# Kernel optimization log

Measured on AMD Instinct MI355X. Metric: run time of the kernel, lower is better.

The kernel has to match this reference:

```python
import jax, jax.numpy as jnp
import numpy as np

PATCH_LEN = 16
D_MODEL = 512


def setup_inputs() -> dict:
    key = jax.random.key(0)
    k_x, k_w1, k_b1, k_w2, k_b2 = jax.random.split(key, 5)
    x = jax.random.normal(k_x, (8, 32, 512), dtype=jnp.float32)
    # Filter_Generators: Linear(patch_len -> d_model), ReLU, Linear(d_model -> patch_len*d_model), ReLU
    s1 = 1.0 / np.sqrt(PATCH_LEN)
    s2 = 1.0 / np.sqrt(D_MODEL)
    W1 = jax.random.uniform(k_w1, (PATCH_LEN, D_MODEL), jnp.float32, -s1, s1)
    b1 = jax.random.uniform(k_b1, (D_MODEL,), jnp.float32, -s1, s1)
    W2 = jax.random.uniform(k_w2, (D_MODEL, PATCH_LEN * D_MODEL), jnp.float32, -s2, s2)
    b2 = jax.random.uniform(k_b2, (PATCH_LEN * D_MODEL,), jnp.float32, -s2, s2)
    return {"x": x, "W1": W1, "b1": b1, "W2": W2, "b2": b2}


def reference(x, W1, b1, W2, b2):
    B = x.shape[0]
    # reshape to patches: (B, N, patch_len)
    xp = x.reshape(B, -1, PATCH_LEN)
    N = xp.shape[1]
    # dynamic filter generation MLP
    h = jax.nn.relu(jnp.einsum('bnp,pd->bnd', xp, W1) + b1)          # (B,N,D)
    filt = jax.nn.relu(jnp.einsum('bnd,de->bne', h, W2) + b2)        # (B,N,P*D)
    # softmax over the sequence (N) axis, per channel (dim=-2 in torch)
    filt = jax.nn.softmax(filt, axis=1)
    filt = filt.reshape(B, N, D_MODEL, PATCH_LEN)                    # (B,N,D,P)
    # broadcast multiply with input patches
    out = filt * xp[:, :, None, :]                                   # (B,N,D,P)
    out = out.transpose(0, 1, 3, 2).reshape(B, N * PATCH_LEN, D_MODEL)
    # AvgPool1d(kernel=3, stride=1, padding=1, count_include_pad=True) over last dim
    p = jnp.pad(out, ((0, 0), (0, 0), (1, 1)))
    out = (p[..., :-2] + p[..., 1:-1] + p[..., 2:]) * (1.0 / 3.0)
    return out
```

## Files before the change

### kernel.cpp

```cpp
#include <hip/hip_runtime.h>
#include <stdint.h>

typedef __attribute__((ext_vector_type(8))) short short8;
typedef __attribute__((ext_vector_type(4))) float floatx4;
typedef unsigned short ushort_t;

__device__ __forceinline__ ushort_t f2bf(float f) {
    union { float f; unsigned int i; } v; v.f = f;
    unsigned int r = v.i + 0x7fffu + ((v.i >> 16) & 1u);
    return (ushort_t)(r >> 16);
}


__global__ __launch_bounds__(256) void k_prep(
    const float* __restrict__ W2, ushort_t* __restrict__ W2T)
{
    __shared__ float t[32][33];
    const int tid = threadIdx.x;
    const int tx = tid & 31, ty = tid >> 5;
    const int e0 = blockIdx.x * 32, k0 = blockIdx.y * 32;
#pragma unroll
    for (int i = 0; i < 4; ++i)
        t[ty + i * 8][tx] = W2[(size_t)(k0 + ty + i * 8) * 8192 + e0 + tx];
    __syncthreads();
#pragma unroll
    for (int i = 0; i < 4; ++i)
        W2T[(size_t)(e0 + ty + i * 8) * 512 + k0 + tx] = f2bf(t[tx][ty + i * 8]);
}

__global__ __launch_bounds__(256) void k1_hidden(
    const float* __restrict__ x, const float* __restrict__ W1,
    const float* __restrict__ b1, ushort_t* __restrict__ h)
{
    __shared__ float xs[16];
    const int r = blockIdx.x;
    const int tid = threadIdx.x;
    if (tid < 16) xs[tid] = x[r * 16 + tid];
    __syncthreads();
#pragma unroll
    for (int dd = 0; dd < 2; ++dd) {
        int d = tid + dd * 256;
        float s = b1[d];
#pragma unroll
        for (int p = 0; p < 16; ++p)
            s += xs[p] * W1[p * 512 + d];
        s = s > 0.f ? s : 0.f;
        h[(size_t)r * 512 + d] = f2bf(s);
    }
}

__global__ __launch_bounds__(256) void k2_sums(
    const ushort_t* __restrict__ h,
    const ushort_t* __restrict__ W2T,
    const float* __restrict__ b2,
    float* __restrict__ P)
{
    __shared__ __align__(16) ushort_t As[128 * 32];
    __shared__ __align__(16) ushort_t Bs[128 * 32];
    __shared__ float csum[128];
    const int tid = threadIdx.x;
    const int lane = tid & 63;
    const int wave = tid >> 6;
    const int quad = lane >> 4;
    const int l16 = lane & 15;
    const int i0 = blockIdx.x * 128;
    const int e0 = blockIdx.y * 128;
    const int wr = (wave >> 1) * 64;
    const int wc = (wave & 1) * 64;

    if (tid < 128) csum[tid] = 0.f;

    floatx4 acc[4][4];
#pragma unroll
    for (int i = 0; i < 4; ++i)
#pragma unroll
        for (int j = 0; j < 4; ++j)
            acc[i][j] = (floatx4){0.f, 0.f, 0.f, 0.f};

    for (int k0 = 0; k0 < 512; k0 += 32) {
#pragma unroll
        for (int s = 0; s < 2; ++s) {
            int q = tid + s * 256;
            int row = q >> 2;
            int c = q & 3;
            uint4 va = *reinterpret_cast<const uint4*>(&h[(size_t)(i0 + row) * 512 + k0 + c * 8]);
            uint4 vb = *reinterpret_cast<const uint4*>(&W2T[(size_t)(e0 + row) * 512 + k0 + c * 8]);
            *reinterpret_cast<uint4*>(&As[row * 32 + ((c ^ (row & 3)) << 3)]) = va;
            *reinterpret_cast<uint4*>(&Bs[row * 32 + ((c ^ (row & 3)) << 3)]) = vb;
        }
        __syncthreads();
        short8 af[4], bf[4];
#pragma unroll
        for (int i = 0; i < 4; ++i) {
            int m = wr + i * 16 + l16;
            af[i] = *reinterpret_cast<const short8*>(&As[m * 32 + ((quad ^ (m & 3)) << 3)]);
            int n = wc + i * 16 + l16;
            bf[i] = *reinterpret_cast<const short8*>(&Bs[n * 32 + ((quad ^ (n & 3)) << 3)]);
        }
#pragma unroll
        for (int i = 0; i < 4; ++i)
#pragma unroll
            for (int j = 0; j < 4; ++j)
                acc[i][j] = __builtin_amdgcn_mfma_f32_16x16x32_bf16(af[i], bf[j], acc[i][j], 0, 0, 0);
        __syncthreads();
    }

#pragma unroll
    for (int j = 0; j < 4; ++j) {
        int eg = e0 + wc + j * 16 + l16;
        float b2v = b2[eg];
        float csj = 0.f;
#pragma unroll
        for (int i = 0; i < 4; ++i)
#pragma unroll
            for (int r = 0; r < 4; ++r) {
                float v = acc[i][j][r] + b2v;
                v = v > 0.f ? v : 0.f;
                csj += __expf(v);
            }
        csj += __shfl_xor(csj, 16, 64);
        csj += __shfl_xor(csj, 32, 64);
        if (lane < 16) atomicAdd(&csum[wc + j * 16 + l16], csj);
    }
    __syncthreads();
    if (tid < 128) P[(size_t)blockIdx.x * 8192 + e0 + tid] = csum[tid];
}

__global__ __launch_bounds__(256) void k_rdenom(const float* __restrict__ P,
                                                float* __restrict__ rden)
{
    int idx = blockIdx.x * 256 + threadIdx.x;
    int b = idx >> 13;
    int e = idx & 8191;
    float s = 0.f;
#pragma unroll
    for (int j = 0; j < 8; ++j) s += P[(size_t)(b * 8 + j) * 8192 + e];
    rden[idx] = 1.0f / s;
}

__global__ __launch_bounds__(256) void k2_final(
    const ushort_t* __restrict__ h,
    const ushort_t* __restrict__ W2T,
    const float* __restrict__ b2,
    const float* __restrict__ x,
    const float* __restrict__ rden,
    float* __restrict__ out)
{
    __shared__ __align__(16) ushort_t As[128 * 32];
    __shared__ __align__(16) ushort_t Bs[160 * 32];
    __shared__ float xs[128 * 17];
    const int tid = threadIdx.x;
    const int lane = tid & 63;
    const int wave = tid >> 6;
    const int quad = lane >> 4;
    const int l16 = lane & 15;
    const int i0 = blockIdx.x * 128;
    const int d0 = blockIdx.y * 8;
    const int ebase = blockIdx.y * 128 - 16;
    const int wrow = wave * 32;
    const int b = i0 >> 10;

#pragma unroll
    for (int s = 0; s < 8; ++s) {
        int q = tid + s * 256;
        xs[(q >> 4) * 17 + (q & 15)] = x[(size_t)(i0 + (q >> 4)) * 16 + (q & 15)];
    }

    floatx4 acc[2][10];
#pragma unroll
    for (int i = 0; i < 2; ++i)
#pragma unroll
        for (int t = 0; t < 10; ++t)
            acc[i][t] = (floatx4){0.f, 0.f, 0.f, 0.f};

    for (int k0 = 0; k0 < 512; k0 += 32) {
#pragma unroll
        for (int s = 0; s < 2; ++s) {
            int q = tid + s * 256;
            int row = q >> 2, c = q & 3;
            uint4 va = *reinterpret_cast<const uint4*>(&h[(size_t)(i0 + row) * 512 + k0 + c * 8]);
            *reinterpret_cast<uint4*>(&As[row * 32 + ((c ^ (row & 3)) << 3)]) = va;
        }
#pragma unroll
        for (int s = 0; s < 3; ++s) {
            int q = tid + s * 256;
            if (q < 640) {
                int row = q >> 2, c = q & 3;
                int eg = ebase + row;
                eg = eg < 0 ? 0 : (eg > 8191 ? 8191 : eg);
                uint4 vb = *reinterpret_cast<const uint4*>(&W2T[(size_t)eg * 512 + k0 + c * 8]);
                *reinterpret_cast<uint4*>(&Bs[row * 32 + ((c ^ (row & 3)) << 3)]) = vb;
            }
        }
        __syncthreads();
        short8 af[2], bf[10];
#pragma unroll
        for (int i = 0; i < 2; ++i) {
            int m = wrow + i * 16 + l16;
            af[i] = *reinterpret_cast<const short8*>(&As[m * 32 + ((quad ^ (m & 3)) << 3)]);
        }
#pragma unroll
        for (int t = 0; t < 10; ++t) {
            int n = t * 16 + l16;
            bf[t] = *reinterpret_cast<const short8*>(&Bs[n * 32 + ((quad ^ (n & 3)) << 3)]);
        }
#pragma unroll
        for (int i = 0; i < 2; ++i)
#pragma unroll
            for (int t = 0; t < 10; ++t)
                acc[i][t] = __builtin_amdgcn_mfma_f32_16x16x32_bf16(af[i], bf[t], acc[i][t], 0, 0, 0);
        __syncthreads();
    }

#pragma unroll
    for (int t = 0; t < 10; ++t) {
        int el = t * 16 + l16;
        int eg = ebase + el;
        int valid = (eg >= 0) & (eg < 8192);
        int egc = valid ? eg : 0;
        float b2v = b2[egc];
        float scale = valid ? rden[b * 8192 + egc] : 0.f;
#pragma unroll
        for (int i = 0; i < 2; ++i) {
            int rbase = wrow + i * 16 + quad * 4;
#pragma unroll
            for (int r = 0; r < 4; ++r) {
                float v = acc[i][t][r] + b2v;
                v = v > 0.f ? v : 0.f;
                acc[i][t][r] = __expf(v) * scale * xs[(rbase + r) * 17 + l16];
            }
        }
    }

    const float inv3 = 1.f / 3.f;
#pragma unroll
    for (int i = 0; i < 2; ++i) {
        int rbase = wrow + i * 16 + quad * 4;
#pragma unroll
        for (int r = 0; r < 4; ++r) {
            int row = rbase + r;
            float g0 = acc[i][0][r], g1 = acc[i][1][r], g2 = acc[i][2][r];
            float g3 = acc[i][3][r], g4 = acc[i][4][r], g5 = acc[i][5][r];
            float g6 = acc[i][6][r], g7 = acc[i][7][r], g8 = acc[i][8][r];
            float g9 = acc[i][9][r];
            float4 o1, o2;
            o1.x = (g0 + g1 + g2) * inv3;
            o1.y = (g1 + g2 + g3) * inv3;
            o1.z = (g2 + g3 + g4) * inv3;
            o1.w = (g3 + g4 + g5) * inv3;
            o2.x = (g4 + g5 + g6) * inv3;
            o2.y = (g5 + g6 + g7) * inv3;
            o2.z = (g6 + g7 + g8) * inv3;
            o2.w = (g7 + g8 + g9) * inv3;
            size_t orow = (size_t)((i0 + row) * 16 + l16);
            *reinterpret_cast<float4*>(&out[orow * 512 + d0]) = o1;
            *reinterpret_cast<float4*>(&out[orow * 512 + d0 + 4]) = o2;
        }
    }
}

extern "C" void kernel_launch(void* const* d_in, const int* in_sizes, int n_in,
                              void* d_out, int out_size, void* d_ws, size_t ws_size,
                              hipStream_t stream)
{
    const float* x  = (const float*)d_in[0];
    const float* W1 = (const float*)d_in[1];
    const float* b1 = (const float*)d_in[2];
    const float* W2 = (const float*)d_in[3];
    const float* b2 = (const float*)d_in[4];
    float* out = (float*)d_out;

    char* ws = (char*)d_ws;
    ushort_t* h    = (ushort_t*)(ws);
    ushort_t* W2T  = (ushort_t*)(ws + (size_t)(8u << 20));
    float*    rden = (float*)(ws + (size_t)(16u << 20));
    float*    P    = (float*)d_out;

    k_prep<<<dim3(256, 16), 256, 0, stream>>>(W2, W2T);
    k1_hidden<<<8192, 256, 0, stream>>>(x, W1, b1, h);
    k2_sums<<<dim3(64, 64), 256, 0, stream>>>(h, W2T, b2, P);
    k_rdenom<<<256, 256, 0, stream>>>(P, rden);
    k2_final<<<dim3(64, 64), 256, 0, stream>>>(h, W2T, b2, x, rden, out);
}
```

Baseline: 597.5 us.

## Double-buffer LDS tiles in both GEMM kernels and load x into registers

Both MFMA GEMM kernels (k2_sums and k2_final) now use two LDS buffers. The next K-tile's global loads are issued into registers before the current tile's MFMAs and written to the other buffer afterwards, which leaves one barrier per iteration. The goal is to hide global load latency behind compute. k2_final also drops its xs shared array and reads x values straight into registers after the main loop. The cost is twice the LDS footprint, which may reduce occupancy, plus more register pressure from the staged loads.

After: 584.9 us. -2.1%, faster.

```diff
diff --git a/kernel.cpp b/kernel.cpp
--- a/kernel.cpp
+++ b/kernel.cpp
@@ -55,8 +55,8 @@
     const float* __restrict__ b2,
     float* __restrict__ P)
 {
-    __shared__ __align__(16) ushort_t As[128 * 32];
-    __shared__ __align__(16) ushort_t Bs[128 * 32];
+    __shared__ __align__(16) ushort_t As[2][128 * 32];
+    __shared__ __align__(16) ushort_t Bs[2][128 * 32];
     __shared__ float csum[128];
     const int tid = threadIdx.x;
     const int lane = tid & 63;
@@ -70,6 +70,16 @@
 
     if (tid < 128) csum[tid] = 0.f;
 
+    const int q0 = tid, q1 = tid + 256;
+    const int row0 = q0 >> 2, c0 = q0 & 3;
+    const int row1 = q1 >> 2, c1 = q1 & 3;
+    const int w0 = row0 * 32 + ((c0 ^ (row0 & 3)) << 3);
+    const int w1 = row1 * 32 + ((c1 ^ (row1 & 3)) << 3);
+    const ushort_t* gA0 = &h[(size_t)(i0 + row0) * 512 + c0 * 8];
+    const ushort_t* gA1 = &h[(size_t)(i0 + row1) * 512 + c1 * 8];
+    const ushort_t* gB0 = &W2T[(size_t)(e0 + row0) * 512 + c0 * 8];
+    const ushort_t* gB1 = &W2T[(size_t)(e0 + row1) * 512 + c1 * 8];
+
     floatx4 acc[4][4];
 #pragma unroll
     for (int i = 0; i < 4; ++i)
@@ -77,32 +87,47 @@
         for (int j = 0; j < 4; ++j)
             acc[i][j] = (floatx4){0.f, 0.f, 0.f, 0.f};
 
-    for (int k0 = 0; k0 < 512; k0 += 32) {
-#pragma unroll
-        for (int s = 0; s < 2; ++s) {
-            int q = tid + s * 256;
-            int row = q >> 2;
-            int c = q & 3;
-            uint4 va = *reinterpret_cast<const uint4*>(&h[(size_t)(i0 + row) * 512 + k0 + c * 8]);
-            uint4 vb = *reinterpret_cast<const uint4*>(&W2T[(size_t)(e0 + row) * 512 + k0 + c * 8]);
-            *reinterpret_cast<uint4*>(&As[row * 32 + ((c ^ (row & 3)) << 3)]) = va;
-            *reinterpret_cast<uint4*>(&Bs[row * 32 + ((c ^ (row & 3)) << 3)]) = vb;
-        }
-        __syncthreads();
-        short8 af[4], bf[4];
+    uint4 a0 = *reinterpret_cast<const uint4*>(gA0);
+    uint4 a1 = *reinterpret_cast<const uint4*>(gA1);
+    uint4 b0 = *reinterpret_cast<const uint4*>(gB0);
+    uint4 b1 = *reinterpret_cast<const uint4*>(gB1);
+    *reinterpret_cast<uint4*>(&As[0][w0]) = a0;
+    *reinterpret_cast<uint4*>(&As[0][w1]) = a1;
+    *reinterpret_cast<uint4*>(&Bs[0][w0]) = b0;
+    *reinterpret_cast<uint4*>(&Bs[0][w1]) = b1;
+    __syncthreads();
+
+    int cur = 0;
+    for (int kt = 0; kt < 16; ++kt) {
+        uint4 na0, na1, nb0, nb1;
+        if (kt < 15) {
+            int k0 = (kt + 1) * 32;
+            na0 = *reinterpret_cast<const uint4*>(gA0 + k0);
+            na1 = *reinterpret_cast<const uint4*>(gA1 + k0);
+            nb0 = *reinterpret_cast<const uint4*>(gB0 + k0);
+            nb1 = *reinterpret_cast<const uint4*>(gB1 + k0);
+        }
+        short8 af[4], bfr[4];
 #pragma unroll
         for (int i = 0; i < 4; ++i) {
             int m = wr + i * 16 + l16;
-            af[i] = *reinterpret_cast<const short8*>(&As[m * 32 + ((quad ^ (m & 3)) << 3)]);
+            af[i] = *reinterpret_cast<const short8*>(&As[cur][m * 32 + ((quad ^ (m & 3)) << 3)]);
             int n = wc + i * 16 + l16;
-            bf[i] = *reinterpret_cast<const short8*>(&Bs[n * 32 + ((quad ^ (n & 3)) << 3)]);
+            bfr[i] = *reinterpret_cast<const short8*>(&Bs[cur][n * 32 + ((quad ^ (n & 3)) << 3)]);
         }
 #pragma unroll
         for (int i = 0; i < 4; ++i)
 #pragma unroll
             for (int j = 0; j < 4; ++j)
-                acc[i][j] = __builtin_amdgcn_mfma_f32_16x16x32_bf16(af[i], bf[j], acc[i][j], 0, 0, 0);
+                acc[i][j] = __builtin_amdgcn_mfma_f32_16x16x32_bf16(af[i], bfr[j], acc[i][j], 0, 0, 0);
+        if (kt < 15) {
+            *reinterpret_cast<uint4*>(&As[cur ^ 1][w0]) = na0;
+            *reinterpret_cast<uint4*>(&As[cur ^ 1][w1]) = na1;
+            *reinterpret_cast<uint4*>(&Bs[cur ^ 1][w0]) = nb0;
+            *reinterpret_cast<uint4*>(&Bs[cur ^ 1][w1]) = nb1;
+        }
         __syncthreads();
+        cur ^= 1;
     }
 
 #pragma unroll
@@ -146,9 +171,8 @@
     const float* __restrict__ rden,
     float* __restrict__ out)
 {
-    __shared__ __align__(16) ushort_t As[128 * 32];
-    __shared__ __align__(16) ushort_t Bs[160 * 32];
-    __shared__ float xs[128 * 17];
+    __shared__ __align__(16) ushort_t As[2][128 * 32];
+    __shared__ __align__(16) ushort_t Bs[2][160 * 32];
     const int tid = threadIdx.x;
     const int lane = tid & 63;
     const int wave = tid >> 6;
@@ -160,11 +184,22 @@
     const int wrow = wave * 32;
     const int b = i0 >> 10;
 
-#pragma unroll
-    for (int s = 0; s < 8; ++s) {
-        int q = tid + s * 256;
-        xs[(q >> 4) * 17 + (q & 15)] = x[(size_t)(i0 + (q >> 4)) * 16 + (q & 15)];
-    }
+    const int q0 = tid, q1 = tid + 256, q2 = tid + 512;
+    const int row0 = q0 >> 2, c0 = q0 & 3;
+    const int row1 = q1 >> 2, c1 = q1 & 3;
+    const int row2 = q2 >> 2, c2 = q2 & 3;
+    const bool act2 = q2 < 640;
+    const int w0 = row0 * 32 + ((c0 ^ (row0 & 3)) << 3);
+    const int w1 = row1 * 32 + ((c1 ^ (row1 & 3)) << 3);
+    const int w2 = row2 * 32 + ((c2 ^ (row2 & 3)) << 3);
+    int ebr0 = ebase + row0; ebr0 = ebr0 < 0 ? 0 : (ebr0 > 8191 ? 8191 : ebr0);
+    int ebr1 = ebase + row1; ebr1 = ebr1 < 0 ? 0 : (ebr1 > 8191 ? 8191 : ebr1);
+    int ebr2 = ebase + row2; ebr2 = ebr2 < 0 ? 0 : (ebr2 > 8191 ? 8191 : ebr2);
+    const ushort_t* gA0 = &h[(size_t)(i0 + row0) * 512 + c0 * 8];
+    const ushort_t* gA1 = &h[(size_t)(i0 + row1) * 512 + c1 * 8];
+    const ushort_t* gB0 = &W2T[(size_t)ebr0 * 512 + c0 * 8];
+    const ushort_t* gB1 = &W2T[(size_t)ebr1 * 512 + c1 * 8];
+    const ushort_t* gB2 = &W2T[(size_t)ebr2 * 512 + c2 * 8];
 
     floatx4 acc[2][10];
 #pragma unroll
@@ -173,44 +208,66 @@
         for (int t = 0; t < 10; ++t)
             acc[i][t] = (floatx4){0.f, 0.f, 0.f, 0.f};
 
-    for (int k0 = 0; k0 < 512; k0 += 32) {
-#pragma unroll
-        for (int s = 0; s < 2; ++s) {
-            int q = tid + s * 256;
-            int row = q >> 2, c = q & 3;
-            uint4 va = *reinterpret_cast<const uint4*>(&h[(size_t)(i0 + row) * 512 + k0 + c * 8]);
-            *reinterpret_cast<uint4*>(&As[row * 32 + ((c ^ (row & 3)) << 3)]) = va;
-        }
-#pragma unroll
-        for (int s = 0; s < 3; ++s) {
-            int q = tid + s * 256;
-            if (q < 640) {
-                int row = q >> 2, c = q & 3;
-                int eg = ebase + row;
-                eg = eg < 0 ? 0 : (eg > 8191 ? 8191 : eg);
-                uint4 vb = *reinterpret_cast<const uint4*>(&W2T[(size_t)eg * 512 + k0 + c * 8]);
-                *reinterpret_cast<uint4*>(&Bs[row * 32 + ((c ^ (row & 3)) << 3)]) = vb;
-            }
-        }
-        __syncthreads();
-        short8 af[2], bf[10];
+    {
+        uint4 a0 = *reinterpret_cast<const uint4*>(gA0);
+        uint4 a1 = *reinterpret_cast<const uint4*>(gA1);
+        uint4 b0 = *reinterpret_cast<const uint4*>(gB0);
+        uint4 b1 = *reinterpret_cast<const uint4*>(gB1);
+        *reinterpret_cast<uint4*>(&As[0][w0]) = a0;
+        *reinterpret_cast<uint4*>(&As[0][w1]) = a1;
+        *reinterpret_cast<uint4*>(&Bs[0][w0]) = b0;
+        *reinterpret_cast<uint4*>(&Bs[0][w1]) = b1;
+        if (act2) {
+            uint4 b2c = *reinterpret_cast<const uint4*>(gB2);
+            *reinterpret_cast<uint4*>(&Bs[0][w2]) = b2c;
+        }
+    }
+    __syncthreads();
+
+    int cur = 0;
+    for (int kt = 0; kt < 16; ++kt) {
+        uint4 na0, na1, nb0, nb1, nb2;
+        if (kt < 15) {
+            int k0 = (kt + 1) * 32;
+            na0 = *reinterpret_cast<const uint4*>(gA0 + k0);
+            na1 = *reinterpret_cast<const uint4*>(gA1 + k0);
+            nb0 = *reinterpret_cast<const uint4*>(gB0 + k0);
+            nb1 = *reinterpret_cast<const uint4*>(gB1 + k0);
+            if (act2) nb2 = *reinterpret_cast<const uint4*>(gB2 + k0);
+        }
+        short8 af[2], bfr[10];
 #pragma unroll
         for (int i = 0; i < 2; ++i) {
             int m = wrow + i * 16 + l16;
-            af[i] = *reinterpret_cast<const short8*>(&As[m * 32 + ((quad ^ (m & 3)) << 3)]);
+            af[i] = *reinterpret_cast<const short8*>(&As[cur][m * 32 + ((quad ^ (m & 3)) << 3)]);
         }
 #pragma unroll
         for (int t = 0; t < 10; ++t) {
             int n = t * 16 + l16;
-            bf[t] = *reinterpret_cast<const short8*>(&Bs[n * 32 + ((quad ^ (n & 3)) << 3)]);
+            bfr[t] = *reinterpret_cast<const short8*>(&Bs[cur][n * 32 + ((quad ^ (n & 3)) << 3)]);
         }
 #pragma unroll
         for (int i = 0; i < 2; ++i)
 #pragma unroll
             for (int t = 0; t < 10; ++t)
-                acc[i][t] = __builtin_amdgcn_mfma_f32_16x16x32_bf16(af[i], bf[t], acc[i][t], 0, 0, 0);
+                acc[i][t] = __builtin_amdgcn_mfma_f32_16x16x32_bf16(af[i], bfr[t], acc[i][t], 0, 0, 0);
+        if (kt < 15) {
+            *reinterpret_cast<uint4*>(&As[cur ^ 1][w0]) = na0;
+            *reinterpret_cast<uint4*>(&As[cur ^ 1][w1]) = na1;
+            *reinterpret_cast<uint4*>(&Bs[cur ^ 1][w0]) = nb0;
+            *reinterpret_cast<uint4*>(&Bs[cur ^ 1][w1]) = nb1;
+            if (act2) *reinterpret_cast<uint4*>(&Bs[cur ^ 1][w2]) = nb2;
+        }
         __syncthreads();
-    }
+        cur ^= 1;
+    }
+
+    float xv[8];
+#pragma unroll
+    for (int i = 0; i < 2; ++i)
+#pragma unroll
+        for (int r = 0; r < 4; ++r)
+            xv[i * 4 + r] = x[(size_t)(i0 + wrow + i * 16 + quad * 4 + r) * 16 + l16];
 
 #pragma unroll
     for (int t = 0; t < 10; ++t) {
@@ -222,12 +279,11 @@
         float scale = valid ? rden[b * 8192 + egc] : 0.f;
 #pragma unroll
         for (int i = 0; i < 2; ++i) {
-            int rbase = wrow + i * 16 + quad * 4;
 #pragma unroll
             for (int r = 0; r < 4; ++r) {
                 float v = acc[i][t][r] + b2v;
                 v = v > 0.f ? v : 0.f;
-                acc[i][t][r] = __expf(v) * scale * xs[(rbase + r) * 17 + l16];
+                acc[i][t][r] = __expf(v) * scale * xv[i * 4 + r];
             }
         }
     }
```
